# Kernel tuning notes

Hardware: AMD Instinct MI355X
Metric: run time of the kernel (lower is better)

## Reference

```python
import jax, jax.numpy as jnp
import numpy as np

B, T, I, H, O = 128, 512, 256, 512, 256


def setup_inputs() -> dict:
    key = jax.random.key(0)
    ks = jax.random.split(key, 12)
    s = 1.0 / np.sqrt(H)  # torch nn.GRUCell/Linear-style uniform init scale
    u = lambda k, shape: jax.random.uniform(k, shape, jnp.float32, -s, s)
    return {
        "x": jax.random.normal(ks[0], (B, T, I), jnp.float32),
        "h0": jax.random.normal(ks[1], (B, H), jnp.float32),
        "W_ih0": u(ks[2], (3 * H, I)),
        "W_hh0": u(ks[3], (3 * H, H)),
        "b_ih0": u(ks[4], (3 * H,)),
        "b_hh0": u(ks[5], (3 * H,)),
        "W_ih1": u(ks[6], (3 * H, H)),
        "W_hh1": u(ks[7], (3 * H, H)),
        "b_ih1": u(ks[8], (3 * H,)),
        "b_hh1": u(ks[9], (3 * H,)),
        "W_out": u(ks[10], (O, H)),
        "b_out": u(ks[11], (O,)),
    }


def _cell(inp, h, W_ih, W_hh, b_ih, b_hh):
    # Standard GRU cell (PyTorch gate order: r, z, n)
    gi = inp @ W_ih.T + b_ih  # [B, 3H]
    gh = h @ W_hh.T + b_hh    # [B, 3H]
    i_r, i_z, i_n = jnp.split(gi, 3, axis=-1)
    h_r, h_z, h_n = jnp.split(gh, 3, axis=-1)
    r = jax.nn.sigmoid(i_r + h_r)
    z = jax.nn.sigmoid(i_z + h_z)
    n = jnp.tanh(i_n + r * h_n)
    return (1.0 - z) * n + z * h


def reference(x, h0, W_ih0, W_hh0, b_ih0, b_hh0, W_ih1, W_hh1, b_ih1, b_hh1, W_out, b_out):
    def step(h, x_t):
        h = _cell(x_t, h, W_ih0, W_hh0, b_ih0, b_hh0)
        # Source quirk: a SINGLE hidden state is shared across stacked layers,
        # so layer 1 receives h both as input and as previous hidden state.
        h = _cell(h, h, W_ih1, W_hh1, b_ih1, b_hh1)
        y = h @ W_out.T + b_out  # [B, O]
        return h, y

    _, Y = jax.lax.scan(step, h0, jnp.swapaxes(x, 0, 1))  # Y: [T, B, O]
    return jnp.swapaxes(Y, 0, 1)  # [B, T, O]
```

## Files before the change

### kernel.cpp

```cpp
#include <hip/hip_runtime.h>


typedef short s16x8 __attribute__((ext_vector_type(8)));
typedef float f32x4 __attribute__((ext_vector_type(4)));
typedef unsigned short u16;
typedef unsigned int u32;

#define MFMA(a, b, c) __builtin_amdgcn_mfma_f32_16x16x32_bf16((a), (b), (c), 0, 0, 0)

static constexpr int NBLK = 128;
static constexpr int LDS_WROWS = 112;
static constexpr int LDS_STRIDE = 520;
static constexpr int LDS_BYTES = LDS_WROWS * LDS_STRIDE * 2 + 2 * 512 * 4;
static constexpr int OFF_FA = 0;
static constexpr int OFF_FB = 8192;
static constexpr int OFF_GA = 16384;
static constexpr int OFF_GB = 18432;
static constexpr int FLAGS_U32 = 20480;

__device__ __forceinline__ u16 f2bf(float f) {
  unsigned u = __builtin_bit_cast(unsigned, f);
  u = u + 0x7fffu + ((u >> 16) & 1u);
  return (u16)(u >> 16);
}
__device__ __forceinline__ float sigm(float x) { return 1.f / (1.f + __expf(-x)); }
__device__ __forceinline__ float tanh_f(float x) { return 1.f - 2.f / (1.f + __expf(2.f * x)); }

__device__ __forceinline__ s16x8 scload16(const u16* p) {
  s16x8 v;
  asm volatile("global_load_dwordx4 %0, %1, off sc0 sc1" : "=v"(v) : "v"(p));
  return v;
}
__device__ __forceinline__ void scstore_u16(u16* p, u16 v) {
  unsigned vv = v;
  asm volatile("global_store_short %0, %1, off sc0 sc1" :: "v"(p), "v"(vv) : "memory");
}
__device__ __forceinline__ u32 scload_u32(const u32* p) {
  u32 v;
  asm volatile("global_load_dword %0, %1, off sc0 sc1\n\ts_waitcnt vmcnt(0)"
               : "=v"(v) : "v"(p) : "memory");
  return v;
}
__device__ __forceinline__ void scstore_u32(u32* p, u32 v) {
  asm volatile("global_store_dword %0, %1, off sc0 sc1" :: "v"(p), "v"(v) : "memory");
}
#define VWAIT0()                                        \
  do {                                                  \
    asm volatile("s_waitcnt vmcnt(0)" ::: "memory");    \
    __builtin_amdgcn_sched_barrier(0);                  \
  } while (0)
#define DRAIN_ALL()                                              \
  do {                                                           \
    asm volatile("s_waitcnt vmcnt(0) lgkmcnt(0)" ::: "memory");  \
    __builtin_amdgcn_sched_barrier(0);                           \
  } while (0)

__device__ __forceinline__ void gather32(const u32* base, u32 val, int l) {
  for (;;) {
    int ok = 1;
    if (l < 32) {
      u32 v = scload_u32(base + l * 32);
      ok = (v >= val) ? 1 : 0;
    }
    if (__all(ok)) break;
    __builtin_amdgcn_s_sleep(2);
  }
}
__device__ __forceinline__ void pollgo(const u32* p, u32 val) {
  for (;;) {
    u32 v = scload_u32(p);
    if (v >= val) break;
    __builtin_amdgcn_s_sleep(2);
  }
}

__global__ void prep_kernel(const float* __restrict__ W_ih0, const float* __restrict__ W_hh0,
                            const float* __restrict__ W_ih1, const float* __restrict__ W_hh1,
                            const float* __restrict__ W_out, const float* __restrict__ h0,
                            u16* __restrict__ WL0, u16* __restrict__ WL1,
                            u16* __restrict__ WOB, u16* __restrict__ ring1,
                            u32* __restrict__ flags) {
  const int n0 = 1536 * 768, n1 = 2048 * 512, n2 = 256 * 512, n3 = 128 * 512;
  const int total = n0 + n1 + n2 + n3 + FLAGS_U32;
  for (int i = blockIdx.x * blockDim.x + threadIdx.x; i < total; i += gridDim.x * blockDim.x) {
    if (i < n0) {
      int row = i / 768, c = i % 768;
      float v = (c < 256) ? W_ih0[row * 256 + c] : W_hh0[row * 512 + (c - 256)];
      WL0[i] = f2bf(v);
    } else if (i < n0 + n1) {
      int k2 = i - n0;
      int row = k2 / 512, k = k2 % 512;
      int strip = row >> 9, j = row & 511;
      float v;
      if (strip == 0)      v = W_ih1[j * 512 + k] + W_hh1[j * 512 + k];
      else if (strip == 1) v = W_ih1[(512 + j) * 512 + k] + W_hh1[(512 + j) * 512 + k];
      else if (strip == 2) v = W_ih1[(1024 + j) * 512 + k];
      else                 v = W_hh1[(1024 + j) * 512 + k];
      WL1[k2] = f2bf(v);
    } else if (i < n0 + n1 + n2) {
      int k2 = i - n0 - n1;
      WOB[k2] = f2bf(W_out[k2]);
    } else if (i < n0 + n1 + n2 + n3) {
      int k2 = i - n0 - n1 - n2;
      ring1[k2] = f2bf(h0[k2]);
    } else {
      flags[i - n0 - n1 - n2 - n3] = 0u;
    }
  }
}

__global__ __launch_bounds__(256) void gru_persist(
    const float* __restrict__ x, const float* __restrict__ h0,
    const float* __restrict__ b_ih0, const float* __restrict__ b_hh0,
    const float* __restrict__ b_ih1, const float* __restrict__ b_hh1,
    const float* __restrict__ b_out,
    const u16* __restrict__ WL0, const u16* __restrict__ WL1, const u16* __restrict__ WOB,
    u16* __restrict__ ring,
    u16* __restrict__ hlb,
    float* __restrict__ Y, u32* __restrict__ flags) {
  extern __shared__ u16 smem[];
  float* h_f32  = (float*)(smem + LDS_WROWS * LDS_STRIDE);
  float* hl_f32 = h_f32 + 512;

  const int blk = blockIdx.x;
  const int m = blk >> 5;
  const int s = blk & 31;
  const int w = threadIdx.x >> 6, l = threadIdx.x & 63;
  const int l15 = l & 15, l4 = l >> 4;

  for (int idx = threadIdx.x; idx < LDS_WROWS * 512; idx += 256) {
    int row = idx >> 9, k = idx & 511;
    u16 v;
    if (row < 48) {
      int g = row >> 4, jj = row & 15;
      v = WL0[(size_t)(g * 512 + s * 16 + jj) * 768 + 256 + k];
    } else {
      int rr = row - 48, g = rr >> 4, jj = rr & 15;
      v = WL1[(size_t)(g * 512 + s * 16 + jj) * 512 + k];
    }
    smem[row * LDS_STRIDE + k] = v;
  }
  for (int idx = threadIdx.x; idx < 512; idx += 256) {
    int rr = idx >> 4, cc = idx & 15;
    h_f32[idx] = h0[(size_t)(32 * m + rr) * 512 + s * 16 + cc];
  }
  __syncthreads();

  const int jg = s * 16 + l15;
  const float br0 = b_ih0[jg] + b_hh0[jg];
  const float bz0 = b_ih0[512 + jg] + b_hh0[512 + jg];
  const float bni0 = b_ih0[1024 + jg], bnh0 = b_hh0[1024 + jg];
  const float br1 = b_ih1[jg] + b_hh1[jg];
  const float bz1 = b_ih1[512 + jg] + b_hh1[512 + jg];
  const float bni1 = b_ih1[1024 + jg], bnh1 = b_hh1[1024 + jg];

  const u16* wxr = WL0 + (size_t)jg * 768 + l4 * 8;
  const u16* wxz = WL0 + (size_t)(512 + jg) * 768 + l4 * 8;
  const u16* wxn = WL0 + (size_t)(1024 + jg) * 768 + l4 * 8;
  const u16* lr  = smem + (0 * 16 + l15) * LDS_STRIDE + l4 * 8;
  const u16* lz  = smem + (1 * 16 + l15) * LDS_STRIDE + l4 * 8;
  const u16* ln  = smem + (2 * 16 + l15) * LDS_STRIDE + l4 * 8;
  const u16* m10 = smem + (48 + 0 * 16 + l15) * LDS_STRIDE + l4 * 8;
  const u16* m11 = smem + (48 + 1 * 16 + l15) * LDS_STRIDE + l4 * 8;
  const u16* m12 = smem + (48 + 2 * 16 + l15) * LDS_STRIDE + l4 * 8;
  const u16* m13 = smem + (48 + 3 * 16 + l15) * LDS_STRIDE + l4 * 8;

  if (w < 2) {
    const int tl = w;
    const int arow = 32 * m + tl * 16 + l15;
    u32* fAt = flags + OFF_FA + (m * 2 + tl) * 1024;
    u32* fBt = flags + OFF_FB + (m * 2 + tl) * 1024;
    u32* gBt = flags + OFF_GB + (m * 2 + tl) * 256;
    u32* myfA = fAt + s * 32;
    const u32* mygo = gBt + (s & 7) * 32;
    const int yo = (s & 15) * 16 + l15;
    const float ybo = b_out[yo];
    const u16* ywv = WOB + (size_t)yo * 512 + l4 * 8;

    for (int t = 0; t < 512; ++t) {
      const u16* ringc = ring + (size_t)((t + 1) & 1) * 65536;

      if (t > 0) {
        if (s == 0) {
          gather32(fBt, (u32)t, l);
          if (l < 8) scstore_u32(gBt + l * 32, (u32)t);
        } else {
          pollgo(mygo, (u32)t);
        }
        __builtin_amdgcn_sched_barrier(0);
      }

      s16x8 hb[16];
      const u16* hr = ringc + (size_t)arow * 512 + l4 * 8;
      #pragma unroll
      for (int kt = 0; kt < 16; ++kt) hb[kt] = scload16(hr + kt * 32);

      f32x4 aR = {0,0,0,0}, aZ = {0,0,0,0}, aNI = {0,0,0,0}, aNH = {0,0,0,0};
      const float* xr = x + ((size_t)arow * 512 + t) * 256 + l4 * 8;
      #pragma unroll
      for (int kt = 0; kt < 8; ++kt) {
        float4 u = *(const float4*)(xr + kt * 32);
        float4 v = *(const float4*)(xr + kt * 32 + 4);
        s16x8 a;
        a[0]=f2bf(u.x); a[1]=f2bf(u.y); a[2]=f2bf(u.z); a[3]=f2bf(u.w);
        a[4]=f2bf(v.x); a[5]=f2bf(v.y); a[6]=f2bf(v.z); a[7]=f2bf(v.w);
        aR  = MFMA(a, *(const s16x8*)(wxr + kt * 32), aR);
        aZ  = MFMA(a, *(const s16x8*)(wxz + kt * 32), aZ);
        aNI = MFMA(a, *(const s16x8*)(wxn + kt * 32), aNI);
      }
      VWAIT0();
      #pragma unroll
      for (int kt = 0; kt < 16; ++kt) {
        aR  = MFMA(hb[kt], *(const s16x8*)(lr + kt * 32), aR);
        aZ  = MFMA(hb[kt], *(const s16x8*)(lz + kt * 32), aZ);
        aNH = MFMA(hb[kt], *(const s16x8*)(ln + kt * 32), aNH);
      }

      #pragma unroll
      for (int j = 0; j < 4; ++j) {
        int rr = tl * 16 + l4 * 4 + j;
        float r = sigm(aR[j] + br0), z = sigm(aZ[j] + bz0);
        float n = tanh_f(aNI[j] + bni0 + r * (aNH[j] + bnh0));
        float h = (1.f - z) * n + z * h_f32[rr * 16 + l15];
        hl_f32[rr * 16 + l15] = h;
        scstore_u16(hlb + (size_t)(32 * m + rr) * 512 + jg, f2bf(h));
      }

      f32x4 yacc = {0,0,0,0};
      if (s < 16 && t > 0) {
        #pragma unroll
        for (int kt = 0; kt < 16; ++kt)
          yacc = MFMA(hb[kt], *(const s16x8*)(ywv + kt * 32), yacc);
      }
      DRAIN_ALL();
      if (l == 0) scstore_u32(myfA, (u32)(t + 1));

      if (s < 16 && t > 0) {
        #pragma unroll
        for (int j = 0; j < 4; ++j)
          Y[((size_t)(32 * m + tl * 16 + l4 * 4 + j) * 512 + (t - 1)) * 256 + yo]
              = yacc[j] + ybo;
      }
    }

    if (s == 0) {
      gather32(fBt, 512u, l);
      if (l < 8) scstore_u32(gBt + l * 32, 512u);
    } else {
      pollgo(mygo, 512u);
    }
    if (s < 16) {
      const u16* Hf = ring + 65536;
      s16x8 yb[16];
      const u16* ar = Hf + (size_t)arow * 512 + l4 * 8;
      #pragma unroll
      for (int kt = 0; kt < 16; ++kt) yb[kt] = scload16(ar + kt * 32);
      VWAIT0();
      f32x4 acc = {0,0,0,0};
      #pragma unroll
      for (int kt = 0; kt < 16; ++kt)
        acc = MFMA(yb[kt], *(const s16x8*)(ywv + kt * 32), acc);
      #pragma unroll
      for (int j = 0; j < 4; ++j)
        Y[((size_t)(32 * m + tl * 16 + l4 * 4 + j) * 512 + 511) * 256 + yo]
            = acc[j] + ybo;
    }
  } else {
    const int tl = w - 2;
    const int brow = 32 * m + tl * 16 + l15;
    u32* fAt = flags + OFF_FA + (m * 2 + tl) * 1024;
    u32* fBt = flags + OFF_FB + (m * 2 + tl) * 1024;
    u32* gAt = flags + OFF_GA + (m * 2 + tl) * 256;
    u32* myfB = fBt + s * 32;
    const u32* mygo = gAt + (s & 7) * 32;

    for (int t = 0; t < 512; ++t) {
      u16* ringn = ring + (size_t)(t & 1) * 65536;

      if (s == 0) {
        gather32(fAt, (u32)(t + 1), l);
        if (l < 8) scstore_u32(gAt + l * 32, (u32)(t + 1));
      } else {
        pollgo(mygo, (u32)(t + 1));
      }
      __builtin_amdgcn_sched_barrier(0);

      s16x8 pb[16];
      const u16* ar = hlb + (size_t)brow * 512 + l4 * 8;
      #pragma unroll
      for (int kt = 0; kt < 16; ++kt) pb[kt] = scload16(ar + kt * 32);
      VWAIT0();
      f32x4 cR = {0,0,0,0}, cZ = {0,0,0,0}, cNI = {0,0,0,0}, cNH = {0,0,0,0};
      #pragma unroll
      for (int kt = 0; kt < 16; ++kt) {
        cR  = MFMA(pb[kt], *(const s16x8*)(m10 + kt * 32), cR);
        cZ  = MFMA(pb[kt], *(const s16x8*)(m11 + kt * 32), cZ);
        cNI = MFMA(pb[kt], *(const s16x8*)(m12 + kt * 32), cNI);
        cNH = MFMA(pb[kt], *(const s16x8*)(m13 + kt * 32), cNH);
      }
      #pragma unroll
      for (int j = 0; j < 4; ++j) {
        int rr = tl * 16 + l4 * 4 + j;
        float r = sigm(cR[j] + br1), z = sigm(cZ[j] + bz1);
        float n = tanh_f(cNI[j] + bni1 + r * (cNH[j] + bnh1));
        float h = (1.f - z) * n + z * hl_f32[rr * 16 + l15];
        h_f32[rr * 16 + l15] = h;
        scstore_u16(ringn + (size_t)(32 * m + rr) * 512 + jg, f2bf(h));
      }
      DRAIN_ALL();
      if (l == 0) scstore_u32(myfB, (u32)(t + 1));
    }
  }
}

extern "C" void kernel_launch(void* const* d_in, const int* in_sizes, int n_in,
                              void* d_out, int out_size, void* d_ws, size_t ws_size,
                              hipStream_t stream) {
  const float* x     = (const float*)d_in[0];
  const float* h0    = (const float*)d_in[1];
  const float* W_ih0 = (const float*)d_in[2];
  const float* W_hh0 = (const float*)d_in[3];
  const float* b_ih0 = (const float*)d_in[4];
  const float* b_hh0 = (const float*)d_in[5];
  const float* W_ih1 = (const float*)d_in[6];
  const float* W_hh1 = (const float*)d_in[7];
  const float* b_ih1 = (const float*)d_in[8];
  const float* b_hh1 = (const float*)d_in[9];
  const float* W_out = (const float*)d_in[10];
  const float* b_out = (const float*)d_in[11];
  float* Y = (float*)d_out;

  u32* flags = (u32*)d_ws;
  u16* WL0  = (u16*)(flags + FLAGS_U32);
  u16* WL1  = WL0 + 1536 * 768;
  u16* WOB  = WL1 + 2048 * 512;
  u16* ring = WOB + 256 * 512;
  u16* hlb  = ring + 2 * 65536;

  (void)hipFuncSetAttribute((const void*)gru_persist,
                            hipFuncAttributeMaxDynamicSharedMemorySize, LDS_BYTES);

  prep_kernel<<<dim3(1024), dim3(256), 0, stream>>>(W_ih0, W_hh0, W_ih1, W_hh1,
                                                    W_out, h0, WL0, WL1, WOB,
                                                    ring + 65536, flags);
  gru_persist<<<dim3(NBLK), dim3(256), LDS_BYTES, stream>>>(
      x, h0, b_ih0, b_hh0, b_ih1, b_hh1, b_out, WL0, WL1, WOB,
      ring, hlb, Y, flags);
}
```

Measured before the change: 6.018 ms.

## Replace two-level gather/broadcast flags with direct per-consumer mailbox barriers

The previous barrier had one leader wave gather 32 producer flags and then broadcast a go flag, which every other wave polled. Now each producer writes its step counter into a mailbox slot for every consumer (32 stores), and each consumer polls its own 64-slot region directly with a wave-wide all-check. This takes the leader hop off the critical path of every recurrent step and shortens the sleep interval. In exchange it adds more flag stores per step and a larger flag workspace, and it raises the polling traffic to memory.

```diff
diff --git a/kernel.cpp b/kernel.cpp
--- a/kernel.cpp
+++ b/kernel.cpp
@@ -12,11 +12,9 @@
 static constexpr int LDS_WROWS = 112;
 static constexpr int LDS_STRIDE = 520;
 static constexpr int LDS_BYTES = LDS_WROWS * LDS_STRIDE * 2 + 2 * 512 * 4;
-static constexpr int OFF_FA = 0;
-static constexpr int OFF_FB = 8192;
-static constexpr int OFF_GA = 16384;
-static constexpr int OFF_GB = 18432;
-static constexpr int FLAGS_U32 = 20480;
+static constexpr int OFF_BA = 0;
+static constexpr int OFF_BB = 65536;
+static constexpr int FLAGS_U32 = 131072;
 
 __device__ __forceinline__ u16 f2bf(float f) {
   unsigned u = __builtin_bit_cast(unsigned, f);
@@ -55,22 +53,12 @@
     __builtin_amdgcn_sched_barrier(0);                           \
   } while (0)
 
-__device__ __forceinline__ void gather32(const u32* base, u32 val, int l) {
-  for (;;) {
-    int ok = 1;
-    if (l < 32) {
-      u32 v = scload_u32(base + l * 32);
-      ok = (v >= val) ? 1 : 0;
-    }
-    if (__all(ok)) break;
-    __builtin_amdgcn_s_sleep(2);
-  }
-}
-__device__ __forceinline__ void pollgo(const u32* p, u32 val) {
+__device__ __forceinline__ void pollbox(const u32* region, u32 val, int l) {
+  const u32* p = region + l * 8;
   for (;;) {
     u32 v = scload_u32(p);
-    if (v >= val) break;
-    __builtin_amdgcn_s_sleep(2);
+    if (__all(v >= val)) break;
+    __builtin_amdgcn_s_sleep(1);
   }
 }
 
@@ -165,14 +153,14 @@
   const u16* m12 = smem + (48 + 2 * 16 + l15) * LDS_STRIDE + l4 * 8;
   const u16* m13 = smem + (48 + 3 * 16 + l15) * LDS_STRIDE + l4 * 8;
 
+  u32* boxA = flags + OFF_BA + (size_t)m * 32 * 64 * 8;
+  u32* boxB = flags + OFF_BB + (size_t)m * 32 * 64 * 8;
+
   if (w < 2) {
     const int tl = w;
+    const int pidx = s * 2 + tl;
     const int arow = 32 * m + tl * 16 + l15;
-    u32* fAt = flags + OFF_FA + (m * 2 + tl) * 1024;
-    u32* fBt = flags + OFF_FB + (m * 2 + tl) * 1024;
-    u32* gBt = flags + OFF_GB + (m * 2 + tl) * 256;
-    u32* myfA = fAt + s * 32;
-    const u32* mygo = gBt + (s & 7) * 32;
+    const u32* myregion = boxB + (size_t)s * 64 * 8;
     const int yo = (s & 15) * 16 + l15;
     const float ybo = b_out[yo];
     const u16* ywv = WOB + (size_t)yo * 512 + l4 * 8;
@@ -181,12 +169,7 @@
       const u16* ringc = ring + (size_t)((t + 1) & 1) * 65536;
 
       if (t > 0) {
-        if (s == 0) {
-          gather32(fBt, (u32)t, l);
-          if (l < 8) scstore_u32(gBt + l * 32, (u32)t);
-        } else {
-          pollgo(mygo, (u32)t);
-        }
+        pollbox(myregion, (u32)t, l);
         __builtin_amdgcn_sched_barrier(0);
       }
 
@@ -233,7 +216,7 @@
           yacc = MFMA(hb[kt], *(const s16x8*)(ywv + kt * 32), yacc);
       }
       DRAIN_ALL();
-      if (l == 0) scstore_u32(myfA, (u32)(t + 1));
+      if (l < 32) scstore_u32(boxA + ((size_t)l * 64 + pidx) * 8, (u32)(t + 1));
 
       if (s < 16 && t > 0) {
         #pragma unroll
@@ -243,12 +226,7 @@
       }
     }
 
-    if (s == 0) {
-      gather32(fBt, 512u, l);
-      if (l < 8) scstore_u32(gBt + l * 32, 512u);
-    } else {
-      pollgo(mygo, 512u);
-    }
+    pollbox(myregion, 512u, l);
     if (s < 16) {
       const u16* Hf = ring + 65536;
       s16x8 yb[16];
@@ -267,22 +245,14 @@
     }
   } else {
     const int tl = w - 2;
+    const int pidx = s * 2 + tl;
     const int brow = 32 * m + tl * 16 + l15;
-    u32* fAt = flags + OFF_FA + (m * 2 + tl) * 1024;
-    u32* fBt = flags + OFF_FB + (m * 2 + tl) * 1024;
-    u32* gAt = flags + OFF_GA + (m * 2 + tl) * 256;
-    u32* myfB = fBt + s * 32;
-    const u32* mygo = gAt + (s & 7) * 32;
+    const u32* myregion = boxA + (size_t)s * 64 * 8;
 
     for (int t = 0; t < 512; ++t) {
       u16* ringn = ring + (size_t)(t & 1) * 65536;
 
-      if (s == 0) {
-        gather32(fAt, (u32)(t + 1), l);
-        if (l < 8) scstore_u32(gAt + l * 32, (u32)(t + 1));
-      } else {
-        pollgo(mygo, (u32)(t + 1));
-      }
+      pollbox(myregion, (u32)(t + 1), l);
       __builtin_amdgcn_sched_barrier(0);
 
       s16x8 pb[16];
@@ -308,7 +278,7 @@
         scstore_u16(ringn + (size_t)(32 * m + rr) * 512 + jg, f2bf(h));
       }
       DRAIN_ALL();
-      if (l == 0) scstore_u32(myfB, (u32)(t + 1));
+      if (l < 32) scstore_u32(boxB + ((size_t)l * 64 + pidx) * 8, (u32)(t + 1));
     }
   }
 }
```

After: 6.778 ms. +12.6%, slower.
